# Kernel tuning notes

Measured on AMD Instinct MI355X. Metric: run time of the kernel, lower is better.

## Reference

```python
import jax, jax.numpy as jnp
import numpy as np
import math

B, LT, LS, D, H, DFF = 4, 1024, 1024, 1024, 16, 4096
DK = D // H
EPS = 1e-5


def setup_inputs() -> dict:
    key = jax.random.key(0)
    ks = jax.random.split(key, 32)
    n = lambda i, shape, s=0.02: jax.random.normal(ks[i], shape, jnp.float32) * s
    inp = {
        'tgt': jax.random.normal(ks[0], (B, LT, D), jnp.float32),
        'memory': jax.random.normal(ks[1], (B, LS, D), jnp.float32),
        'src_pad_mask': jnp.zeros((B, LT, LS), dtype=bool),
        'tgt_mask': jnp.broadcast_to(jnp.triu(jnp.ones((LT, LT), dtype=bool), 1), (B, LT, LT)),
        # self-attention projections
        'self_wq': n(2, (D, D)), 'self_bq': jnp.zeros((D,)),
        'self_wk': n(3, (D, D)), 'self_bk': jnp.zeros((D,)),
        'self_wv': n(4, (D, D)), 'self_bv': jnp.zeros((D,)),
        'self_wo': n(5, (D, D)), 'self_bo': jnp.zeros((D,)),
        # cross-attention projections
        'cross_wq': n(6, (D, D)), 'cross_bq': jnp.zeros((D,)),
        'cross_wk': n(7, (D, D)), 'cross_bk': jnp.zeros((D,)),
        'cross_wv': n(8, (D, D)), 'cross_bv': jnp.zeros((D,)),
        'cross_wo': n(9, (D, D)), 'cross_bo': jnp.zeros((D,)),
        # layer norms (pre-norm)
        'ln1_g': jnp.ones((D,)), 'ln1_b': jnp.zeros((D,)),
        'ln2_g': jnp.ones((D,)), 'ln2_b': jnp.zeros((D,)),
        'ln3_g': jnp.ones((D,)), 'ln3_b': jnp.zeros((D,)),
        # feed forward
        'ffn_w1': n(10, (D, DFF)), 'ffn_b1': jnp.zeros((DFF,)),
        'ffn_w2': n(11, (DFF, D)), 'ffn_b2': jnp.zeros((D,)),
    }
    return inp


def _layernorm(x, g, b):
    mu = jnp.mean(x, axis=-1, keepdims=True)
    var = jnp.mean(jnp.square(x - mu), axis=-1, keepdims=True)
    return (x - mu) * jax.lax.rsqrt(var + EPS) * g + b


def _mha(xq, xkv, wq, bq, wk, bk, wv, bv, wo, bo, mask):
    b, lq, d = xq.shape
    lk = xkv.shape[1]
    q = (xq @ wq + bq).reshape(b, lq, H, DK).transpose(0, 2, 1, 3) / math.sqrt(DK)
    k = (xkv @ wk + bk).reshape(b, lk, H, DK).transpose(0, 2, 1, 3)
    v = (xkv @ wv + bv).reshape(b, lk, H, DK).transpose(0, 2, 1, 3)
    scores = jnp.einsum('bhqd,bhkd->bhqk', q, k)  # [B,H,Lq,Lk]
    scores = jnp.where(mask[:, None], -1e18, scores)
    attn = jax.nn.softmax(scores, axis=-1)  # dropout p=0 (eval)
    ctx = jnp.einsum('bhqk,bhkd->bhqd', attn, v)
    ctx = ctx.transpose(0, 2, 1, 3).reshape(b, lq, d)
    return ctx @ wo + bo


def reference(tgt, memory, src_pad_mask, tgt_mask,
              self_wq, self_bq, self_wk, self_bk, self_wv, self_bv, self_wo, self_bo,
              cross_wq, cross_bq, cross_wk, cross_bk, cross_wv, cross_bv, cross_wo, cross_bo,
              ln1_g, ln1_b, ln2_g, ln2_b, ln3_g, ln3_b,
              ffn_w1, ffn_b1, ffn_w2, ffn_b2):
    # pre-norm sublayer 1: self attention
    x = tgt + _mha(_layernorm(tgt, ln1_g, ln1_b), _layernorm(tgt, ln1_g, ln1_b),
                   self_wq, self_bq, self_wk, self_bk, self_wv, self_bv, self_wo, self_bo, tgt_mask)
    # pre-norm sublayer 2: cross attention
    x = x + _mha(_layernorm(x, ln2_g, ln2_b), memory,
                 cross_wq, cross_bq, cross_wk, cross_bk, cross_wv, cross_bv, cross_wo, cross_bo, src_pad_mask)
    # pre-norm sublayer 3: FFN
    h = _layernorm(x, ln3_g, ln3_b)
    x = x + (jax.nn.gelu(h @ ffn_w1 + ffn_b1) @ ffn_w2 + ffn_b2)
    return x
```

## Files before the change

### kernel.cpp

```cpp
#include <hip/hip_runtime.h>

typedef unsigned short u16;
typedef __attribute__((ext_vector_type(8))) __bf16 bf16x8;
typedef __attribute__((ext_vector_type(4))) float floatx4;

__device__ inline float bf2f(u16 u) {
    union { unsigned int i; float f; } x; x.i = ((unsigned int)u) << 16; return x.f;
}
__device__ inline u16 f2bf(float f) {
    __bf16 h = (__bf16)f; return __builtin_bit_cast(unsigned short, h);
}
__device__ inline float load_f(u16 v) { return bf2f(v); }
__device__ inline float load_f(float v) { return v; }

__device__ inline floatx4 mfma_bf16(bf16x8 a, bf16x8 b, floatx4 c) {
    return __builtin_amdgcn_mfma_f32_16x16x32_bf16(a, b, c, 0, 0, 0);
}

__device__ inline float gelu_tanh(float x) {
    float u = 0.7978845608028654f * (x + 0.044715f * x * x * x);
    u = fminf(fmaxf(u, -15.f), 15.f);
    float e = __expf(2.f * u);
    float th = (e - 1.f) / (e + 1.f);
    return 0.5f * x * (1.f + th);
}

__device__ inline void async16(const void* g, void* l) {
    __builtin_amdgcn_global_load_lds(
        (const __attribute__((address_space(1))) unsigned int*)g,
        (__attribute__((address_space(3))) unsigned int*)l, 16, 0, 0);
}

__global__ __launch_bounds__(256)
void detect_dtype(const u16* __restrict__ p, int* __restrict__ flag) {
    int t = threadIdx.x, cnt = 0;
    #pragma unroll
    for (int j = 0; j < 8; ++j) {
        unsigned e = (p[t * 8 + j] >> 7) & 0xFF;
        cnt += (e >= 100 && e <= 140) ? 1 : 0;
    }
    __shared__ int s[256];
    s[t] = cnt; __syncthreads();
    for (int off = 128; off; off >>= 1) { if (t < off) s[t] += s[t + off]; __syncthreads(); }
    if (t == 0) *flag = (s[0] < 1844) ? 1 : 0;
}

__global__ __launch_bounds__(256)
void convert_to_bf16(const void* __restrict__ src, u16* __restrict__ dst, int n,
                     const int* __restrict__ flag) {
    int f = *flag;
    int i = (blockIdx.x * 256 + threadIdx.x) * 4;
    if (i < n) {
        #pragma unroll
        for (int j = 0; j < 4; ++j)
            dst[i + j] = f ? f2bf(((const float*)src)[i + j]) : ((const u16*)src)[i + j];
    }
}

struct VecTab { const void* src[16]; int n[16]; int off[16]; };
__global__ __launch_bounds__(256)
void convert_vecs(VecTab tab, u16* __restrict__ dst, const int* __restrict__ flag) {
    int f = *flag;
    int b = blockIdx.x;
    const void* s = tab.src[b];
    int n = tab.n[b];
    u16* d = dst + tab.off[b];
    for (int i = threadIdx.x; i < n; i += 256)
        d[i] = f ? f2bf(((const float*)s)[i]) : ((const u16*)s)[i];
}

__global__ __launch_bounds__(256)
void init_X(const void* __restrict__ src, float* __restrict__ X, int n,
            const int* __restrict__ flag) {
    int f = *flag;
    int i = (blockIdx.x * 256 + threadIdx.x) * 4;
    if (i < n) {
        #pragma unroll
        for (int j = 0; j < 4; ++j)
            X[i + j] = f ? ((const float*)src)[i + j] : bf2f(((const u16*)src)[i + j]);
    }
}

__global__ __launch_bounds__(256)
void store_out(const float* __restrict__ X, void* __restrict__ out, int n,
               const int* __restrict__ flag) {
    int f = *flag;
    int i = (blockIdx.x * 256 + threadIdx.x) * 4;
    if (i < n) {
        #pragma unroll
        for (int j = 0; j < 4; ++j) {
            float v = X[i + j];
            if (f) ((float*)out)[i + j] = v;
            else   ((u16*)out)[i + j] = f2bf(v);
        }
    }
}

__global__ __launch_bounds__(256)
void transpose_any(const void* __restrict__ src, u16* __restrict__ dst, int R, int C,
                   const int* __restrict__ flag) {
    int f = *flag;
    __shared__ u16 tile[32][33];
    int tx = threadIdx.x & 31, ty = threadIdx.x >> 5;
    int r0 = blockIdx.y * 32, c0 = blockIdx.x * 32;
    #pragma unroll
    for (int i = 0; i < 32; i += 8) {
        size_t idx = (size_t)(r0 + ty + i) * C + c0 + tx;
        tile[ty + i][tx] = f ? f2bf(((const float*)src)[idx]) : ((const u16*)src)[idx];
    }
    __syncthreads();
    #pragma unroll
    for (int i = 0; i < 32; i += 8)
        dst[(size_t)(c0 + ty + i) * R + r0 + tx] = tile[tx][ty + i];
}

template <typename TIN>
__global__ __launch_bounds__(256)
void lnorm(const TIN* __restrict__ Xin, const u16* __restrict__ gg,
           const u16* __restrict__ bb, u16* __restrict__ Y) {
    const int row = blockIdx.x, t = threadIdx.x;
    const TIN* xr = Xin + (size_t)row * 1024;
    float x[4]; float s1 = 0.f, s2 = 0.f;
    #pragma unroll
    for (int i = 0; i < 4; ++i) {
        float v = load_f(xr[i * 256 + t]);
        x[i] = v; s1 += v; s2 += v * v;
    }
    #pragma unroll
    for (int m = 1; m < 64; m <<= 1) { s1 += __shfl_xor(s1, m, 64); s2 += __shfl_xor(s2, m, 64); }
    __shared__ float red[8];
    if ((t & 63) == 0) { red[(t >> 6) * 2] = s1; red[(t >> 6) * 2 + 1] = s2; }
    __syncthreads();
    s1 = red[0] + red[2] + red[4] + red[6];
    s2 = red[1] + red[3] + red[5] + red[7];
    float mu = s1 * (1.f / 1024.f);
    float var = s2 * (1.f / 1024.f) - mu * mu;
    float rs = rsqrtf(var + 1e-5f);
    #pragma unroll
    for (int i = 0; i < 4; ++i) {
        int idx = i * 256 + t;
        float yv = (x[i] - mu) * rs * bf2f(gg[idx]) + bf2f(bb[idx]);
        Y[(size_t)row * 1024 + idx] = f2bf(yv);
    }
}

__global__ __launch_bounds__(256, 2)
void gemm_bt2(const u16* __restrict__ A, const u16* __restrict__ Bt,
              const u16* __restrict__ bias, u16* __restrict__ C,
              float* __restrict__ Xres, int M, int N, int K, int ldc, int epi) {
    __shared__ alignas(16) u16 As[128 * 32];
    __shared__ alignas(16) u16 Bs[128 * 32];
    const int t = threadIdx.x;
    const int lane = t & 63, w = t >> 6;
    const int l15 = lane & 15, quad = lane >> 4;
    const int m0 = blockIdx.y * 128, n0 = blockIdx.x * 128;
    const int wm = (w >> 1) * 64, wn = (w & 1) * 64;
    const int srow = lane >> 2, scol = (lane & 3) * 8;
    const u16* ga = A + (size_t)(m0 + w * 32 + srow) * K + scol;
    const u16* gb = Bt + (size_t)(n0 + w * 32 + srow) * K + scol;
    u16* lA0 = &As[(w * 32) * 32];
    u16* lA1 = &As[(w * 32 + 16) * 32];
    u16* lB0 = &Bs[(w * 32) * 32];
    u16* lB1 = &Bs[(w * 32 + 16) * 32];
    floatx4 acc[4][4] = {};

    for (int k0 = 0; k0 < K; k0 += 32) {
        __syncthreads();
        async16(ga + k0, lA0);
        async16(ga + (size_t)16 * K + k0, lA1);
        async16(gb + k0, lB0);
        async16(gb + (size_t)16 * K + k0, lB1);
        __syncthreads();
        bf16x8 af[4], bfr[4];
        #pragma unroll
        for (int i = 0; i < 4; ++i) {
            af[i]  = *(const bf16x8*)&As[(wm + i * 16 + l15) * 32 + quad * 8];
            bfr[i] = *(const bf16x8*)&Bs[(wn + i * 16 + l15) * 32 + quad * 8];
        }
        #pragma unroll
        for (int mi = 0; mi < 4; ++mi)
            #pragma unroll
            for (int ni = 0; ni < 4; ++ni)
                acc[mi][ni] = mfma_bf16(af[mi], bfr[ni], acc[mi][ni]);
    }

    #pragma unroll
    for (int mi = 0; mi < 4; ++mi) {
        #pragma unroll
        for (int ni = 0; ni < 4; ++ni) {
            int gn = n0 + wn + ni * 16 + l15;
            float bv = bf2f(bias[gn]);
            #pragma unroll
            for (int r = 0; r < 4; ++r) {
                int gm = m0 + wm + mi * 16 + quad * 4 + r;
                float v = acc[mi][ni][r] + bv;
                size_t idx = (size_t)gm * ldc + gn;
                if (epi == 0)      C[idx] = f2bf(v);
                else if (epi == 1) C[idx] = f2bf(gelu_tanh(v));
                else               Xres[idx] += v;
            }
        }
    }
}

__global__ __launch_bounds__(256, 2)
void attn_fwd2(const u16* __restrict__ QKV, u16* __restrict__ CTX, int causal) {
    __shared__ alignas(16) u16 Ks[64 * 72];
    __shared__ alignas(16) u16 Vst[64 * 72];
    __shared__ alignas(16) u16 Sw[4][16 * 72];
    const int t = threadIdx.x;
    const int lane = t & 63, w = t >> 6;
    const int l15 = lane & 15, quad = lane >> 4;
    const int q0 = blockIdx.x * 64, h = blockIdx.y, b = blockIdx.z;
    const int qrow = q0 + w * 16 + l15;
    const u16* qp = QKV + (size_t)(b * 1024 + qrow) * 3072 + h * 64;
    bf16x8 aq0 = *(const bf16x8*)(qp + quad * 8);
    bf16x8 aq1 = *(const bf16x8*)(qp + 32 + quad * 8);
    floatx4 O[4] = {};
    float mo[4], lo[4];
    #pragma unroll
    for (int r = 0; r < 4; ++r) { mo[r] = -1e30f; lo[r] = 0.f; }

    const int skey = t >> 2, snn = t & 3, sd0 = (t & 3) * 16;
    const int swz = skey ^ (snn << 3);
    const int kend = causal ? (q0 + 64) : 1024;
    for (int kt = 0; kt < kend; kt += 64) {
        __syncthreads();
        {
            const u16* kvb = QKV + (size_t)(b * 1024 + kt + skey) * 3072 + h * 64 + sd0;
            bf16x8 k0v = *(const bf16x8*)(kvb + 1024);
            bf16x8 k1v = *(const bf16x8*)(kvb + 1024 + 8);
            *(bf16x8*)&Ks[skey * 72 + sd0] = k0v;
            *(bf16x8*)&Ks[skey * 72 + sd0 + 8] = k1v;
            bf16x8 v0v = *(const bf16x8*)(kvb + 2048);
            bf16x8 v1v = *(const bf16x8*)(kvb + 2048 + 8);
            #pragma unroll
            for (int j = 0; j < 8; ++j) Vst[(sd0 + j) * 72 + swz] = ((u16*)&v0v)[j];
            #pragma unroll
            for (int j = 0; j < 8; ++j) Vst[(sd0 + 8 + j) * 72 + swz] = ((u16*)&v1v)[j];
        }
        __syncthreads();
        floatx4 S[4];
        #pragma unroll
        for (int kg = 0; kg < 4; ++kg) {
            bf16x8 bk0 = *(const bf16x8*)&Ks[(kg * 16 + l15) * 72 + quad * 8];
            bf16x8 bk1 = *(const bf16x8*)&Ks[(kg * 16 + l15) * 72 + 32 + quad * 8];
            floatx4 z = {};
            z = mfma_bf16(aq0, bk0, z);
            z = mfma_bf16(aq1, bk1, z);
            S[kg] = z;
        }
        const bool domask = causal && (kt == q0);
        float al[4];
        #pragma unroll
        for (int r = 0; r < 4; ++r) {
            #pragma unroll
            for (int kg = 0; kg < 4; ++kg) {
                float s = S[kg][r] * 0.125f;
                if (domask) {
                    int kg_glob = kt + kg * 16 + l15;
                    int qg = q0 + w * 16 + quad * 4 + r;
                    if (kg_glob > qg) s = -1e30f;
                }
                S[kg][r] = s;
            }
            float v = fmaxf(fmaxf(S[0][r], S[1][r]), fmaxf(S[2][r], S[3][r]));
            #pragma unroll
            for (int msk = 1; msk < 16; msk <<= 1) v = fmaxf(v, __shfl_xor(v, msk, 64));
            float mn = fmaxf(mo[r], v);
            al[r] = __expf(mo[r] - mn);
            float ssum = 0.f;
            #pragma unroll
            for (int kg = 0; kg < 4; ++kg) {
                float p = __expf(S[kg][r] - mn);
                S[kg][r] = p; ssum += p;
            }
            #pragma unroll
            for (int msk = 1; msk < 16; msk <<= 1) ssum += __shfl_xor(ssum, msk, 64);
            lo[r] = lo[r] * al[r] + ssum;
            mo[r] = mn;
        }
        #pragma unroll
        for (int kg = 0; kg < 4; ++kg)
            #pragma unroll
            for (int r = 0; r < 4; ++r)
                Sw[w][(quad * 4 + r) * 72 + kg * 16 + l15] = f2bf(S[kg][r]);
        #pragma unroll
        for (int g = 0; g < 4; ++g)
            #pragma unroll
            for (int r = 0; r < 4; ++r)
                O[g][r] *= al[r];
        bf16x8 ap0 = *(const bf16x8*)&Sw[w][l15 * 72 + quad * 8];
        bf16x8 ap1 = *(const bf16x8*)&Sw[w][l15 * 72 + 32 + quad * 8];
        #pragma unroll
        for (int g = 0; g < 4; ++g) {
            bf16x8 bv0 = *(const bf16x8*)&Vst[(g * 16 + l15) * 72 + ((quad ^ g) << 3)];
            bf16x8 bv1 = *(const bf16x8*)&Vst[(g * 16 + l15) * 72 + 32 + ((quad ^ g) << 3)];
            O[g] = mfma_bf16(ap0, bv0, O[g]);
            O[g] = mfma_bf16(ap1, bv1, O[g]);
        }
    }
    #pragma unroll
    for (int r = 0; r < 4; ++r) {
        float inv = 1.0f / lo[r];
        int qg = q0 + w * 16 + quad * 4 + r;
        #pragma unroll
        for (int g = 0; g < 4; ++g)
            CTX[(size_t)(b * 1024 + qg) * 1024 + h * 64 + g * 16 + l15] = f2bf(O[g][r] * inv);
    }
}

extern "C" void kernel_launch(void* const* d_in, const int* in_sizes, int n_in,
                              void* d_out, int out_size, void* d_ws, size_t ws_size,
                              hipStream_t stream) {
    const void* tgt_raw    = d_in[0];
    const void* memory_raw = d_in[1];

    char* ws = (char*)d_ws;
    const size_t MiB = 1024 * 1024;
    float* X   = (float*)ws;
    u16* Y     = (u16*)(ws + 16 * MiB);
    u16* QKV   = (u16*)(ws + 24 * MiB);
    u16* CTX   = (u16*)(ws + 48 * MiB);
    u16* H1    = (u16*)(ws + 24 * MiB);
    u16* wt    = (u16*)(ws + 56 * MiB);
    u16* wqkv_s = wt;
    u16* wo_s  = wt + 3 * 1048576;
    u16* wq_c  = wt + 4 * 1048576;
    u16* wkv_c = wt + 5 * 1048576;
    u16* wo_c  = wt + 7 * 1048576;
    u16* w1t   = wt + 8 * 1048576;
    u16* w2t   = wt + 12 * 1048576;
    u16* tgt_c = (u16*)(ws + 88 * MiB);
    u16* mem_c = (u16*)(ws + 96 * MiB);
    u16* vecs  = (u16*)(ws + 104 * MiB);
    int* flag  = (int*)(ws + 105 * MiB);

    dim3 blk(256);
    detect_dtype<<<1, blk, 0, stream>>>((const u16*)tgt_raw, flag);
    convert_to_bf16<<<4096, blk, 0, stream>>>(tgt_raw, tgt_c, 4096 * 1024, flag);
    convert_to_bf16<<<4096, blk, 0, stream>>>(memory_raw, mem_c, 4096 * 1024, flag);

    VecTab tab;
    const int srcIdx[16] = {5, 7, 9, 11, 13, 15, 17, 19, 20, 21, 22, 23, 24, 25, 27, 29};
    const int offs[16]   = {0, 1024, 2048, 3072, 4096, 5120, 6144, 7168,
                            8192, 9216, 10240, 11264, 12288, 13312, 14336, 18432};
    for (int i = 0; i < 16; ++i) {
        tab.src[i] = d_in[srcIdx[i]];
        tab.n[i] = (i == 14) ? 4096 : 1024;
        tab.off[i] = offs[i];
    }
    convert_vecs<<<16, blk, 0, stream>>>(tab, vecs, flag);
    u16* b_qkv_s = vecs;            u16* b_o_s  = vecs + 3072;
    u16* b_q_c   = vecs + 4096;     u16* b_kv_c = vecs + 5120;
    u16* b_o_c   = vecs + 7168;
    u16* g1 = vecs + 8192;  u16* be1 = vecs + 9216;
    u16* g2 = vecs + 10240; u16* be2 = vecs + 11264;
    u16* g3 = vecs + 12288; u16* be3 = vecs + 13312;
    u16* b_ff1 = vecs + 14336; u16* b_ff2 = vecs + 18432;

    dim3 tg32(32, 32);
    transpose_any<<<tg32, blk, 0, stream>>>(d_in[4],  wqkv_s,               1024, 1024, flag);
    transpose_any<<<tg32, blk, 0, stream>>>(d_in[6],  wqkv_s + 1048576,     1024, 1024, flag);
    transpose_any<<<tg32, blk, 0, stream>>>(d_in[8],  wqkv_s + 2 * 1048576, 1024, 1024, flag);
    transpose_any<<<tg32, blk, 0, stream>>>(d_in[10], wo_s,                 1024, 1024, flag);
    transpose_any<<<tg32, blk, 0, stream>>>(d_in[12], wq_c,                 1024, 1024, flag);
    transpose_any<<<tg32, blk, 0, stream>>>(d_in[14], wkv_c,                1024, 1024, flag);
    transpose_any<<<tg32, blk, 0, stream>>>(d_in[16], wkv_c + 1048576,      1024, 1024, flag);
    transpose_any<<<tg32, blk, 0, stream>>>(d_in[18], wo_c,                 1024, 1024, flag);
    transpose_any<<<dim3(128, 32), blk, 0, stream>>>(d_in[26], w1t, 1024, 4096, flag);
    transpose_any<<<dim3(32, 128), blk, 0, stream>>>(d_in[28], w2t, 4096, 1024, flag);

    const int NTOK = 4096;
    init_X<<<4096, blk, 0, stream>>>(tgt_raw, X, NTOK * 1024, flag);

    dim3 g1k(8, 32), g2k(16, 32), g3k(24, 32), g4k(32, 32);
    dim3 ga(16, 16, 4);

    lnorm<u16><<<4096, blk, 0, stream>>>(tgt_c, g1, be1, Y);
    gemm_bt2<<<g3k, blk, 0, stream>>>(Y, wqkv_s, b_qkv_s, QKV, nullptr, NTOK, 3072, 1024, 3072, 0);
    attn_fwd2<<<ga, blk, 0, stream>>>(QKV, CTX, 1);
    gemm_bt2<<<g1k, blk, 0, stream>>>(CTX, wo_s, b_o_s, nullptr, X, NTOK, 1024, 1024, 1024, 2);

    lnorm<float><<<4096, blk, 0, stream>>>(X, g2, be2, Y);
    gemm_bt2<<<g1k, blk, 0, stream>>>(Y, wq_c, b_q_c, QKV, nullptr, NTOK, 1024, 1024, 3072, 0);
    gemm_bt2<<<g2k, blk, 0, stream>>>(mem_c, wkv_c, b_kv_c, QKV + 1024, nullptr, NTOK, 2048, 1024, 3072, 0);
    attn_fwd2<<<ga, blk, 0, stream>>>(QKV, CTX, 0);
    gemm_bt2<<<g1k, blk, 0, stream>>>(CTX, wo_c, b_o_c, nullptr, X, NTOK, 1024, 1024, 1024, 2);

    lnorm<float><<<4096, blk, 0, stream>>>(X, g3, be3, Y);
    gemm_bt2<<<g4k, blk, 0, stream>>>(Y, w1t, b_ff1, H1, nullptr, NTOK, 4096, 1024, 4096, 1);
    gemm_bt2<<<g1k, blk, 0, stream>>>(H1, w2t, b_ff2, nullptr, X, NTOK, 1024, 4096, 1024, 2);

    store_out<<<4096, blk, 0, stream>>>(X, d_out, NTOK * 1024, flag);
}
```

Before: 738.3 us.

## Split-K residual GEMMs with atomic accumulation, fuse tgt conversion, use exp2 softmax

The N=1024 residual-output GEMMs only launched 256 blocks. They now split K across a grid z dimension (2-way for the output projections, 4-way for FFN2) and accumulate into the fp32 residual with atomicAdd, with the bias added only by the z=0 slice. This gives more blocks to fill the GPU, at the cost of atomic traffic and a summation order that is no longer deterministic. The init_X pass is merged into the tgt bf16 conversion, removing one extra read of the input. Attention softmax now uses exp2f with the log2(e) factor folded into the score scale.

```diff
diff --git a/kernel.cpp b/kernel.cpp
--- a/kernel.cpp
+++ b/kernel.cpp
@@ -54,6 +54,23 @@
         #pragma unroll
         for (int j = 0; j < 4; ++j)
             dst[i + j] = f ? f2bf(((const float*)src)[i + j]) : ((const u16*)src)[i + j];
+    }
+}
+
+__global__ __launch_bounds__(256)
+void convert_tgt(const void* __restrict__ src, u16* __restrict__ dst,
+                 float* __restrict__ X, int n, const int* __restrict__ flag) {
+    int f = *flag;
+    int i = (blockIdx.x * 256 + threadIdx.x) * 4;
+    if (i < n) {
+        #pragma unroll
+        for (int j = 0; j < 4; ++j) {
+            float v; u16 hv;
+            if (f) { v = ((const float*)src)[i + j]; hv = f2bf(v); }
+            else   { hv = ((const u16*)src)[i + j]; v = bf2f(hv); }
+            dst[i + j] = hv;
+            X[i + j] = v;
+        }
     }
 }
 
@@ -67,18 +84,6 @@
     u16* d = dst + tab.off[b];
     for (int i = threadIdx.x; i < n; i += 256)
         d[i] = f ? f2bf(((const float*)s)[i]) : ((const u16*)s)[i];
-}
-
-__global__ __launch_bounds__(256)
-void init_X(const void* __restrict__ src, float* __restrict__ X, int n,
-            const int* __restrict__ flag) {
-    int f = *flag;
-    int i = (blockIdx.x * 256 + threadIdx.x) * 4;
-    if (i < n) {
-        #pragma unroll
-        for (int j = 0; j < 4; ++j)
-            X[i + j] = f ? ((const float*)src)[i + j] : bf2f(((const u16*)src)[i + j]);
-    }
 }
 
 __global__ __launch_bounds__(256)
@@ -155,6 +160,8 @@
     const int l15 = lane & 15, quad = lane >> 4;
     const int m0 = blockIdx.y * 128, n0 = blockIdx.x * 128;
     const int wm = (w >> 1) * 64, wn = (w & 1) * 64;
+    const int ksl = K / gridDim.z;
+    const int kb = blockIdx.z * ksl, ke = kb + ksl;
     const int srow = lane >> 2, scol = (lane & 3) * 8;
     const u16* ga = A + (size_t)(m0 + w * 32 + srow) * K + scol;
     const u16* gb = Bt + (size_t)(n0 + w * 32 + srow) * K + scol;
@@ -164,7 +171,7 @@
     u16* lB1 = &Bs[(w * 32 + 16) * 32];
     floatx4 acc[4][4] = {};
 
-    for (int k0 = 0; k0 < K; k0 += 32) {
+    for (int k0 = kb; k0 < ke; k0 += 32) {
         __syncthreads();
         async16(ga + k0, lA0);
         async16(ga + (size_t)16 * K + k0, lA1);
@@ -184,12 +191,13 @@
                 acc[mi][ni] = mfma_bf16(af[mi], bfr[ni], acc[mi][ni]);
     }
 
+    const bool addb = (blockIdx.z == 0);
     #pragma unroll
     for (int mi = 0; mi < 4; ++mi) {
         #pragma unroll
         for (int ni = 0; ni < 4; ++ni) {
             int gn = n0 + wn + ni * 16 + l15;
-            float bv = bf2f(bias[gn]);
+            float bv = addb ? bf2f(bias[gn]) : 0.f;
             #pragma unroll
             for (int r = 0; r < 4; ++r) {
                 int gm = m0 + wm + mi * 16 + quad * 4 + r;
@@ -197,12 +205,13 @@
                 size_t idx = (size_t)gm * ldc + gn;
                 if (epi == 0)      C[idx] = f2bf(v);
                 else if (epi == 1) C[idx] = f2bf(gelu_tanh(v));
-                else               Xres[idx] += v;
+                else               atomicAdd(&Xres[idx], v);
             }
         }
     }
 }
 
+#define SCL2 0.18033688011112042f
 __global__ __launch_bounds__(256, 2)
 void attn_fwd2(const u16* __restrict__ QKV, u16* __restrict__ CTX, int causal) {
     __shared__ alignas(16) u16 Ks[64 * 72];
@@ -256,7 +265,7 @@
         for (int r = 0; r < 4; ++r) {
             #pragma unroll
             for (int kg = 0; kg < 4; ++kg) {
-                float s = S[kg][r] * 0.125f;
+                float s = S[kg][r] * SCL2;
                 if (domask) {
                     int kg_glob = kt + kg * 16 + l15;
                     int qg = q0 + w * 16 + quad * 4 + r;
@@ -268,11 +277,11 @@
             #pragma unroll
             for (int msk = 1; msk < 16; msk <<= 1) v = fmaxf(v, __shfl_xor(v, msk, 64));
             float mn = fmaxf(mo[r], v);
-            al[r] = __expf(mo[r] - mn);
+            al[r] = exp2f(mo[r] - mn);
             float ssum = 0.f;
             #pragma unroll
             for (int kg = 0; kg < 4; ++kg) {
-                float p = __expf(S[kg][r] - mn);
+                float p = exp2f(S[kg][r] - mn);
                 S[kg][r] = p; ssum += p;
             }
             #pragma unroll
@@ -338,7 +347,7 @@
 
     dim3 blk(256);
     detect_dtype<<<1, blk, 0, stream>>>((const u16*)tgt_raw, flag);
-    convert_to_bf16<<<4096, blk, 0, stream>>>(tgt_raw, tgt_c, 4096 * 1024, flag);
+    convert_tgt<<<4096, blk, 0, stream>>>(tgt_raw, tgt_c, X, 4096 * 1024, flag);
     convert_to_bf16<<<4096, blk, 0, stream>>>(memory_raw, mem_c, 4096 * 1024, flag);
 
     VecTab tab;
@@ -372,25 +381,25 @@
     transpose_any<<<dim3(32, 128), blk, 0, stream>>>(d_in[28], w2t, 4096, 1024, flag);
 
     const int NTOK = 4096;
-    init_X<<<4096, blk, 0, stream>>>(tgt_raw, X, NTOK * 1024, flag);
-
     dim3 g1k(8, 32), g2k(16, 32), g3k(24, 32), g4k(32, 32);
+    dim3 g1k_s2(8, 32, 2);
+    dim3 g1k_s4(8, 32, 4);
     dim3 ga(16, 16, 4);
 
     lnorm<u16><<<4096, blk, 0, stream>>>(tgt_c, g1, be1, Y);
     gemm_bt2<<<g3k, blk, 0, stream>>>(Y, wqkv_s, b_qkv_s, QKV, nullptr, NTOK, 3072, 1024, 3072, 0);
     attn_fwd2<<<ga, blk, 0, stream>>>(QKV, CTX, 1);
-    gemm_bt2<<<g1k, blk, 0, stream>>>(CTX, wo_s, b_o_s, nullptr, X, NTOK, 1024, 1024, 1024, 2);
+    gemm_bt2<<<g1k_s2, blk, 0, stream>>>(CTX, wo_s, b_o_s, nullptr, X, NTOK, 1024, 1024, 1024, 2);
 
     lnorm<float><<<4096, blk, 0, stream>>>(X, g2, be2, Y);
     gemm_bt2<<<g1k, blk, 0, stream>>>(Y, wq_c, b_q_c, QKV, nullptr, NTOK, 1024, 1024, 3072, 0);
     gemm_bt2<<<g2k, blk, 0, stream>>>(mem_c, wkv_c, b_kv_c, QKV + 1024, nullptr, NTOK, 2048, 1024, 3072, 0);
     attn_fwd2<<<ga, blk, 0, stream>>>(QKV, CTX, 0);
-    gemm_bt2<<<g1k, blk, 0, stream>>>(CTX, wo_c, b_o_c, nullptr, X, NTOK, 1024, 1024, 1024, 2);
+    gemm_bt2<<<g1k_s2, blk, 0, stream>>>(CTX, wo_c, b_o_c, nullptr, X, NTOK, 1024, 1024, 1024, 2);
 
     lnorm<float><<<4096, blk, 0, stream>>>(X, g3, be3, Y);
     gemm_bt2<<<g4k, blk, 0, stream>>>(Y, w1t, b_ff1, H1, nullptr, NTOK, 4096, 1024, 4096, 1);
-    gemm_bt2<<<g1k, blk, 0, stream>>>(H1, w2t, b_ff2, nullptr, X, NTOK, 1024, 4096, 1024, 2);
+    gemm_bt2<<<g1k_s4, blk, 0, stream>>>(H1, w2t, b_ff2, nullptr, X, NTOK, 1024, 4096, 1024, 2);
 
     store_out<<<4096, blk, 0, stream>>>(X, d_out, NTOK * 1024, flag);
 }
```

Result: no change. 738.9 us (+0.1%).
